# Kernel tuning notes

Hardware: AMD Instinct MI355X
Metric: run time of the kernel (lower is better)

Reference implementation:

```python
import jax, jax.numpy as jnp
import numpy as np

N_NODES = 50000
N_EDGES = 800000
D_IN = 768
D_H = 256
N_CLASSES = 4
N_LAYERS = 3
N_GRAPHS = 64
LN_EPS = 1e-5


def setup_inputs() -> dict:
    key = jax.random.key(0)
    ks = jax.random.split(key, 12)
    x = jax.random.normal(ks[0], (N_NODES, D_IN), dtype=jnp.float32)
    edge_index = jax.random.randint(ks[1], (2, N_EDGES), 0, N_NODES)
    batch = jnp.sort(jax.random.randint(ks[2], (N_NODES,), 0, N_GRAPHS))
    s_in = 1.0 / np.sqrt(D_IN)
    s_h = 1.0 / np.sqrt(D_H)
    W_in = jax.random.normal(ks[3], (D_IN, D_H), jnp.float32) * s_in
    b_in = jnp.zeros((D_H,), jnp.float32)
    convW = jax.random.normal(ks[4], (N_LAYERS, D_H, D_H), jnp.float32) * s_h
    convB = jnp.zeros((N_LAYERS, D_H), jnp.float32)
    lnG = jnp.ones((N_LAYERS, D_H), jnp.float32)
    lnB = jnp.zeros((N_LAYERS, D_H), jnp.float32)
    clsW1 = jax.random.normal(ks[5], (D_H, D_H), jnp.float32) * s_h
    clsB1 = jnp.zeros((D_H,), jnp.float32)
    clsW2 = jax.random.normal(ks[6], (D_H, N_CLASSES), jnp.float32) * s_h
    clsB2 = jnp.zeros((N_CLASSES,), jnp.float32)
    return {"x": x, "edge_index": edge_index, "batch": batch,
            "W_in": W_in, "b_in": b_in, "convW": convW, "convB": convB,
            "lnG": lnG, "lnB": lnB, "clsW1": clsW1, "clsB1": clsB1,
            "clsW2": clsW2, "clsB2": clsB2}


def _layer_norm(h, g, b):
    mu = jnp.mean(h, axis=-1, keepdims=True)
    var = jnp.mean(jnp.square(h - mu), axis=-1, keepdims=True)
    return (h - mu) * jax.lax.rsqrt(var + LN_EPS) * g + b


def reference(x, edge_index, batch, W_in, b_in, convW, convB, lnG, lnB,
              clsW1, clsB1, clsW2, clsB2):
    N = x.shape[0]
    loops = jnp.arange(N)
    src = jnp.concatenate([edge_index[0], loops])  # self-loops (PyG GCNConv default)
    dst = jnp.concatenate([edge_index[1], loops])
    deg = jax.ops.segment_sum(jnp.ones_like(src, dtype=x.dtype), dst, num_segments=N)
    dinv = jax.lax.rsqrt(deg)  # deg >= 1 due to self-loops
    norm = dinv[src] * dinv[dst]  # symmetric GCN normalization per edge

    h = x @ W_in + b_in  # input projection -> [N, D_H]
    for i in range(N_LAYERS):
        m = h @ convW[i]  # transform then propagate
        h_new = jax.ops.segment_sum(m[src] * norm[:, None], dst, num_segments=N) + convB[i]
        h = jax.nn.relu(h_new + h)  # residual (shapes match), then ReLU
        h = _layer_norm(h, lnG[i], lnB[i])
        # dropout: identity (inference mode)

    g = jax.ops.segment_max(h, batch, num_segments=N_GRAPHS)  # global_max_pool
    z = jax.nn.relu(g @ clsW1 + clsB1)
    return z @ clsW2 + clsB2  # [N_GRAPHS, N_CLASSES]
```

## Files before the change

### kernel.cpp

```cpp
#include <hip/hip_runtime.h>
#include <hip/hip_bf16.h>
#include <math.h>

#define NNODES 50000
#define NEDGES 800000
#define DIN 768
#define DH 256
#define NCLS 4
#define NGRAPHS 64
#define SCAN_BLOCKS 196

typedef __bf16 bf16x8 __attribute__((ext_vector_type(8)));
typedef float f32x4 __attribute__((ext_vector_type(4)));

static __device__ __forceinline__ float bf2f(unsigned short u) {
    union { unsigned u32; float f; } v; v.u32 = ((unsigned)u) << 16; return v.f;
}
static __device__ __forceinline__ unsigned short f2bf(float f) {
    union { float f; unsigned u; } v; v.f = f;
    unsigned r = (v.u + 0x7fffu + ((v.u >> 16) & 1u)) >> 16;
    return (unsigned short)r;
}
static __device__ __forceinline__ void unpack8(uint4 u, float* f) {
    f[0] = bf2f((unsigned short)(u.x & 0xffff)); f[1] = bf2f((unsigned short)(u.x >> 16));
    f[2] = bf2f((unsigned short)(u.y & 0xffff)); f[3] = bf2f((unsigned short)(u.y >> 16));
    f[4] = bf2f((unsigned short)(u.z & 0xffff)); f[5] = bf2f((unsigned short)(u.z >> 16));
    f[6] = bf2f((unsigned short)(u.w & 0xffff)); f[7] = bf2f((unsigned short)(u.w >> 16));
}
static __device__ __forceinline__ uint4 pack8f(float4 f0, float4 f1) {
    uint4 u;
    u.x = (unsigned)f2bf(f0.x) | ((unsigned)f2bf(f0.y) << 16);
    u.y = (unsigned)f2bf(f0.z) | ((unsigned)f2bf(f0.w) << 16);
    u.z = (unsigned)f2bf(f1.x) | ((unsigned)f2bf(f1.y) << 16);
    u.w = (unsigned)f2bf(f1.z) | ((unsigned)f2bf(f1.w) << 16);
    return u;
}
static __device__ __forceinline__ void gload_lds16(const void* g, void* l) {
    __builtin_amdgcn_global_load_lds((const __attribute__((address_space(1))) void*)g,
                                     (__attribute__((address_space(3))) void*)l, 16, 0, 0);
}

__global__ void detect_dtype(const unsigned short* __restrict__ x, int* __restrict__ flag) {
    __shared__ int cnt_s;
    if (threadIdx.x == 0) cnt_s = 0;
    __syncthreads();
    int c = 0;
    for (int i = 0; i < 16; ++i) {
        float v = bf2f(x[threadIdx.x * 16 + i]);
        if (!(fabsf(v) < 1e10f)) c++;
    }
    atomicAdd(&cnt_s, c);
    __syncthreads();
    if (threadIdx.x == 0) flag[0] = (cnt_s > 32) ? 1 : 0;
}

static __device__ __forceinline__ unsigned short cload(const void* src, int i, int fp32) {
    return fp32 ? f2bf(((const float*)src)[i]) : ((const unsigned short*)src)[i];
}

__global__ void canon_small(const void* b_in, const void* convB, const void* lnG,
                            const void* lnB, const void* W1, const void* W2,
                            const void* b1, const void* b2,
                            unsigned short* __restrict__ dst, const int* __restrict__ flag) {
    int i = blockIdx.x * 256 + threadIdx.x;
    if (i >= 69380) return;
    const int fp32 = flag[0];
    int j = i;
    if (j < 256)  { dst[i] = cload(b_in, j, fp32); return; }  j -= 256;
    if (j < 768)  { dst[i] = cload(convB, j, fp32); return; } j -= 768;
    if (j < 768)  { dst[i] = cload(lnG, j, fp32); return; }   j -= 768;
    if (j < 768)  { dst[i] = cload(lnB, j, fp32); return; }   j -= 768;
    if (j < 65536){ dst[i] = cload(W1, j, fp32); return; }    j -= 65536;
    if (j < 1024) { dst[i] = cload(W2, j, fp32); return; }    j -= 1024;
    if (j < 256)  { dst[i] = cload(b1, j, fp32); return; }    j -= 256;
    dst[i] = cload(b2, j, fp32);
}

__global__ void transpose_win(const void* __restrict__ src, unsigned short* __restrict__ dst,
                              const int* __restrict__ flag) {
    int idx = blockIdx.x * 256 + threadIdx.x;
    if (idx < DIN * DH) {
        int r = idx / DH, c = idx % DH;
        dst[(size_t)c * DIN + r] = cload(src, idx, flag[0]);
    }
}
__global__ void transpose_convw(const void* __restrict__ src, unsigned short* __restrict__ dst,
                                const int* __restrict__ flag) {
    int idx = blockIdx.x * 256 + threadIdx.x;
    if (idx < 3 * DH * DH) {
        int l = idx >> 16, rc = idx & 65535;
        int r = rc >> 8, c = rc & 255;
        dst[(l << 16) + c * DH + r] = cload(src, idx, flag[0]);
    }
}

__global__ void fill_sentinel(float* out, int n) {
    int i = blockIdx.x * 256 + threadIdx.x;
    if (i < n) out[i] = 1000.0f;
}

__global__ void count_edges(const int* __restrict__ ei, int* __restrict__ cnt) {
    int e = blockIdx.x * 256 + threadIdx.x;
    if (e < NEDGES) atomicAdd(&cnt[ei[NEDGES + e]], 1);
}

__global__ void scan_local(const int* __restrict__ cnt, int* __restrict__ rowptr,
                           int* __restrict__ bsum) {
    __shared__ int tmp[256];
    int i = blockIdx.x * 256 + threadIdx.x;
    int v = (i < NNODES) ? cnt[i] : 0;
    tmp[threadIdx.x] = v;
    __syncthreads();
    for (int off = 1; off < 256; off <<= 1) {
        int a = (threadIdx.x >= off) ? tmp[threadIdx.x - off] : 0;
        __syncthreads();
        tmp[threadIdx.x] += a;
        __syncthreads();
    }
    if (i < NNODES) rowptr[i] = tmp[threadIdx.x] - v;
    if (threadIdx.x == 255) bsum[blockIdx.x] = tmp[255];
}
__global__ void scan_bsum(const int* __restrict__ bsum, int* __restrict__ boff) {
    __shared__ int tmp[256];
    int t = threadIdx.x;
    int v = (t < SCAN_BLOCKS) ? bsum[t] : 0;
    tmp[t] = v;
    __syncthreads();
    for (int off = 1; off < 256; off <<= 1) {
        int a = (t >= off) ? tmp[t - off] : 0;
        __syncthreads();
        tmp[t] += a;
        __syncthreads();
    }
    if (t < SCAN_BLOCKS) boff[t] = tmp[t] - v;
}
__global__ void scan_finish(int* __restrict__ rowptr, const int* __restrict__ boff,
                            const int* __restrict__ cnt, float* __restrict__ dinv) {
    int i = blockIdx.x * 256 + threadIdx.x;
    if (i < NNODES) {
        rowptr[i] += boff[blockIdx.x];
        dinv[i] = rsqrtf((float)(1 + cnt[i]));
    }
    if (i == 0) rowptr[NNODES] = NEDGES;
}

__global__ void fill_csr(const int* __restrict__ ei, const int* __restrict__ rowptr,
                         int* __restrict__ cursor, int* __restrict__ csrc) {
    int e = blockIdx.x * 256 + threadIdx.x;
    if (e < NEDGES) {
        int s = ei[e];
        int d = ei[NEDGES + e];
        int pos = rowptr[d] + atomicAdd(&cursor[d], 1);
        csrc[pos] = s;
    }
}

#define GBM 64
#define GBN 256
#define GBK 32

__global__ __launch_bounds__(256, 3) void gemm_bf16_tn(
    const void* __restrict__ Araw, const int* __restrict__ dflag, int use_flag,
    const unsigned short* __restrict__ Bt, const unsigned short* __restrict__ bias,
    unsigned short* __restrict__ C, int M, int N, int K)
{
    __shared__ __align__(16) unsigned short As[2][GBM * GBK];
    __shared__ __align__(16) unsigned short Bs[2][GBN * GBK];

    const int a_fp32 = use_flag ? dflag[0] : 0;
    const int m0 = blockIdx.x * GBM;
    const int t = threadIdx.x;
    const int wave = t >> 6, lane = t & 63;
    const int quad = lane >> 4, l16 = lane & 15;
    const int qs8 = (quad ^ ((l16 >> 1) & 3)) * 8;

    const int ar = t >> 2;
    const int ap_ = t & 3;
    const int al = ap_ ^ ((ar >> 1) & 3);
    const bool arow_ok = (m0 + ar) < M;
    const float* abase_f = (const float*)Araw + (size_t)(m0 + ar) * K + al * 8;
    const unsigned short* abase_h = (const unsigned short*)Araw + (size_t)(m0 + ar) * K + al * 8;

    const char* bsrcb[4];
#pragma unroll
    for (int li = 0; li < 4; ++li) {
        int c = wave * 256 + li * 64 + lane;
        int r = c >> 2, p = c & 3;
        int l = p ^ ((r >> 1) & 3);
        bsrcb[li] = (const char*)Bt + ((size_t)r * K + l * 8) * 2;
    }

    f32x4 acc[4][4];
#pragma unroll
    for (int i = 0; i < 4; i++)
#pragma unroll
        for (int j = 0; j < 4; j++) acc[i][j] = (f32x4){0.f, 0.f, 0.f, 0.f};

    {
#pragma unroll
        for (int li = 0; li < 4; ++li)
            gload_lds16(bsrcb[li], &Bs[0][(wave * 256 + li * 64) * 8]);
        uint4 av = make_uint4(0u, 0u, 0u, 0u);
        if (arow_ok) {
            if (a_fp32) {
                float4 f0 = *(const float4*)abase_f;
                float4 f1 = *(const float4*)(abase_f + 4);
                av = pack8f(f0, f1);
            } else {
                av = *(const uint4*)abase_h;
            }
        }
        *(uint4*)(&As[0][t * 8]) = av;
    }
    __syncthreads();

    const int nt = K / GBK;
    for (int tt = 0; tt < nt; ++tt) {
        const int buf = tt & 1;
        const bool hn = (tt + 1) < nt;
        uint4 av = make_uint4(0u, 0u, 0u, 0u);
        float4 f0 = make_float4(0.f, 0.f, 0.f, 0.f);
        float4 f1 = make_float4(0.f, 0.f, 0.f, 0.f);
        if (hn) {
            const int kk = (tt + 1) * GBK;
#pragma unroll
            for (int li = 0; li < 4; ++li)
                gload_lds16(bsrcb[li] + (size_t)kk * 2,
                            &Bs[buf ^ 1][(wave * 256 + li * 64) * 8]);
            if (arow_ok) {
                if (a_fp32) {
                    f0 = *(const float4*)(abase_f + kk);
                    f1 = *(const float4*)(abase_f + kk + 4);
                } else {
                    av = *(const uint4*)(abase_h + kk);
                }
            }
        }
        const unsigned short* as_ = As[buf];
        const unsigned short* bs_ = Bs[buf];
        bf16x8 afv[4], bfv[4];
#pragma unroll
        for (int i = 0; i < 4; i++)
            afv[i] = *(const bf16x8*)(as_ + (16 * i + l16) * 32 + qs8);
#pragma unroll
        for (int j = 0; j < 4; j++)
            bfv[j] = *(const bf16x8*)(bs_ + (wave * 64 + 16 * j + l16) * 32 + qs8);
#pragma unroll
        for (int i = 0; i < 4; i++)
#pragma unroll
            for (int j = 0; j < 4; j++)
                acc[i][j] = __builtin_amdgcn_mfma_f32_16x16x32_bf16(afv[i], bfv[j], acc[i][j], 0, 0, 0);
        if (hn) {
            if (a_fp32 && arow_ok) av = pack8f(f0, f1);
            *(uint4*)(&As[buf ^ 1][t * 8]) = av;
        }
        __syncthreads();
    }

#pragma unroll
    for (int j = 0; j < 4; j++) {
        const int gc = wave * 64 + 16 * j + l16;
        const float bv = bias ? bf2f(bias[gc]) : 0.f;
#pragma unroll
        for (int i = 0; i < 4; i++) {
#pragma unroll
            for (int rr = 0; rr < 4; rr++) {
                int gr = m0 + 16 * i + quad * 4 + rr;
                if (gr < M) C[(size_t)gr * N + gc] = f2bf(acc[i][j][rr] + bv);
            }
        }
    }
}

__global__ __launch_bounds__(256) void aggregate_ln(
    const int* __restrict__ rowptr, const int* __restrict__ csrc,
    const float* __restrict__ dinv, const unsigned short* __restrict__ m,
    const unsigned short* __restrict__ convB,
    const unsigned short* __restrict__ lnG, const unsigned short* __restrict__ lnB,
    unsigned short* __restrict__ h)
{
    const int half = threadIdx.x >> 5;
    const int lane = threadIdx.x & 31;
    const int node = blockIdx.x * 8 + half;
    const float di = dinv[node];
    const size_t base = (size_t)node * DH + lane * 8;
    const size_t lo = lane * 8;

    float v0[8], v1[8], v2[8], v3[8];
    unpack8(*(const uint4*)(m + base), v0);
    const float selfn = di * di;
#pragma unroll
    for (int j = 0; j < 8; j++) { v0[j] *= selfn; v1[j] = 0.f; v2[j] = 0.f; v3[j] = 0.f; }

    const int kb = rowptr[node], ke = rowptr[node + 1];
    int k = kb;
    for (; k + 4 <= ke; k += 4) {
        const int s0 = csrc[k], s1 = csrc[k + 1], s2 = csrc[k + 2], s3 = csrc[k + 3];
        const uint4 r0 = *(const uint4*)(m + (size_t)s0 * DH + lo);
        const uint4 r1 = *(const uint4*)(m + (size_t)s1 * DH + lo);
        const uint4 r2 = *(const uint4*)(m + (size_t)s2 * DH + lo);
        const uint4 r3 = *(const uint4*)(m + (size_t)s3 * DH + lo);
        const float n0 = dinv[s0] * di, n1 = dinv[s1] * di;
        const float n2 = dinv[s2] * di, n3 = dinv[s3] * di;
        float t0[8], t1[8], t2[8], t3[8];
        unpack8(r0, t0); unpack8(r1, t1); unpack8(r2, t2); unpack8(r3, t3);
#pragma unroll
        for (int j = 0; j < 8; j++) {
            v0[j] += t0[j] * n0;
            v1[j] += t1[j] * n1;
            v2[j] += t2[j] * n2;
            v3[j] += t3[j] * n3;
        }
    }
    for (; k < ke; ++k) {
        const int s = csrc[k];
        const uint4 r = *(const uint4*)(m + (size_t)s * DH + lo);
        const float n = dinv[s] * di;
        float tv[8];
        unpack8(r, tv);
#pragma unroll
        for (int j = 0; j < 8; j++) v0[j] += tv[j] * n;
    }
#pragma unroll
    for (int j = 0; j < 8; j++) v0[j] += (v1[j] + v2[j]) + v3[j];

    float hv[8], cv[8];
    unpack8(*(const uint4*)(h + base), hv);
    unpack8(*(const uint4*)(convB + lo), cv);
    float s1 = 0.f, s2 = 0.f;
#pragma unroll
    for (int j = 0; j < 8; j++) {
        v0[j] = fmaxf(v0[j] + cv[j] + hv[j], 0.f);
        s1 += v0[j];
        s2 += v0[j] * v0[j];
    }
#pragma unroll
    for (int off = 16; off > 0; off >>= 1) {
        s1 += __shfl_xor(s1, off, 32);
        s2 += __shfl_xor(s2, off, 32);
    }
    const float mu = s1 * (1.f / 256.f);
    const float var = s2 * (1.f / 256.f) - mu * mu;
    const float rs = rsqrtf(var + 1e-5f);
    float gv[8], bv[8];
    unpack8(*(const uint4*)(lnG + lo), gv);
    unpack8(*(const uint4*)(lnB + lo), bv);
    unsigned short o[8];
#pragma unroll
    for (int j = 0; j < 8; j++) o[j] = f2bf((v0[j] - mu) * rs * gv[j] + bv[j]);
    uint4 outp;
    outp.x = (unsigned)o[0] | ((unsigned)o[1] << 16);
    outp.y = (unsigned)o[2] | ((unsigned)o[3] << 16);
    outp.z = (unsigned)o[4] | ((unsigned)o[5] << 16);
    outp.w = (unsigned)o[6] | ((unsigned)o[7] << 16);
    *(uint4*)(h + base) = outp;
}

__global__ void find_bounds(const int* __restrict__ batch, int* __restrict__ s) {
    int i = blockIdx.x * 256 + threadIdx.x;
    if (i >= NNODES) return;
    int b = batch[i];
    int bp = (i == 0) ? -1 : batch[i - 1];
    for (int g = bp + 1; g <= b; ++g) s[g] = i;
    if (i == NNODES - 1)
        for (int g = b + 1; g <= NGRAPHS; ++g) s[g] = NNODES;
}

#define PSPLIT 8
__global__ __launch_bounds__(256) void pool_partial(
    const unsigned short* __restrict__ h, const int* __restrict__ s,
    float* __restrict__ pg)
{
    const int b = blockIdx.x >> 3, split = blockIdx.x & 7, f = threadIdx.x;
    const int i0 = s[b], i1 = s[b + 1];
    const int len = i1 - i0;
    const int c0 = i0 + (int)(((long)len * split) >> 3);
    const int c1 = i0 + (int)(((long)len * (split + 1)) >> 3);
    float mx = -INFINITY;
    for (int i = c0; i < c1; ++i) mx = fmaxf(mx, bf2f(h[(size_t)i * DH + f]));
    pg[(size_t)blockIdx.x * DH + f] = mx;
}
__global__ __launch_bounds__(256) void pool_reduce(const float* __restrict__ pg,
                                                   float* __restrict__ g) {
    const int b = blockIdx.x, f = threadIdx.x;
    float mx = -INFINITY;
#pragma unroll
    for (int j = 0; j < PSPLIT; ++j) mx = fmaxf(mx, pg[(size_t)(b * PSPLIT + j) * DH + f]);
    g[b * DH + f] = mx;
}

__global__ __launch_bounds__(256) void classifier(
    const float* __restrict__ g, const unsigned short* __restrict__ W1,
    const unsigned short* __restrict__ b1, const unsigned short* __restrict__ W2,
    const unsigned short* __restrict__ b2, void* __restrict__ outv,
    const int* __restrict__ flag)
{
    __shared__ float gz[DH];
    __shared__ float zz[DH];
    const int b = blockIdx.x, t = threadIdx.x;
    gz[t] = g[b * DH + t];
    __syncthreads();
    float s = bf2f(b1[t]);
    for (int k = 0; k < DH; ++k) s += gz[k] * bf2f(W1[k * DH + t]);
    zz[t] = fmaxf(s, 0.f);
    __syncthreads();
    if (t < NCLS) {
        float s2 = bf2f(b2[t]);
        for (int k = 0; k < DH; ++k) s2 += zz[k] * bf2f(W2[k * NCLS + t]);
        if (flag[0]) ((float*)outv)[b * NCLS + t] = s2;
        else ((unsigned short*)outv)[b * NCLS + t] = f2bf(s2);
    }
}

extern "C" void kernel_launch(void* const* d_in, const int* in_sizes, int n_in,
                              void* d_out, int out_size, void* d_ws, size_t ws_size,
                              hipStream_t stream)
{
    const void* x      = d_in[0];
    const int* ei      = (const int*)d_in[1];
    const int* batch   = (const int*)d_in[2];
    const void* Win    = d_in[3];
    const void* b_in   = d_in[4];
    const void* convW  = d_in[5];
    const void* convB  = d_in[6];
    const void* lnG    = d_in[7];
    const void* lnB    = d_in[8];
    const void* W1     = d_in[9];
    const void* b1     = d_in[10];
    const void* W2     = d_in[11];
    const void* b2     = d_in[12];

    char* ws = (char*)d_ws;
    unsigned short* h   = (unsigned short*)(ws + 0);
    unsigned short* m   = (unsigned short*)(ws + 25600000);
    int* csrc           = (int*)(ws + 51200000);
    int* rowptr         = (int*)(ws + 54400000);
    int* cnt            = (int*)(ws + 54600016);
    int* cursor         = (int*)(ws + 54800016);
    float* dinv         = (float*)(ws + 55000016);
    unsigned short* cw  = (unsigned short*)(ws + 55200016);
    unsigned short* WinT= (unsigned short*)(ws + 55338784);
    unsigned short* WcT = (unsigned short*)(ws + 55732000);
    float* g            = (float*)(ws + 56125216);
    float* pg           = (float*)(ws + 56190752);
    int* gb             = (int*)(ws + 56715040);
    int* bsum           = (int*)(ws + 56715312);
    int* boff           = (int*)(ws + 56716112);
    int* flag           = (int*)(ws + 56716912);
    const size_t NEED   = 56716928;
    if (ws_size < NEED) {
        fill_sentinel<<<(out_size / 2 + 255) / 256, 256, 0, stream>>>((float*)d_out, out_size / 2);
        return;
    }

    unsigned short* cBin   = cw + 0;
    unsigned short* cConvB = cw + 256;
    unsigned short* cLnG   = cw + 1024;
    unsigned short* cLnB   = cw + 1792;
    unsigned short* cW1    = cw + 2560;
    unsigned short* cW2    = cw + 68096;
    unsigned short* cB1    = cw + 69120;
    unsigned short* cB2    = cw + 69376;

    detect_dtype<<<1, 256, 0, stream>>>((const unsigned short*)x, flag);

    hipMemsetAsync(cnt, 0, 400000, stream);
    count_edges<<<(NEDGES + 255) / 256, 256, 0, stream>>>(ei, cnt);
    scan_local<<<SCAN_BLOCKS, 256, 0, stream>>>(cnt, rowptr, bsum);
    scan_bsum<<<1, 256, 0, stream>>>(bsum, boff);
    scan_finish<<<SCAN_BLOCKS, 256, 0, stream>>>(rowptr, boff, cnt, dinv);
    fill_csr<<<(NEDGES + 255) / 256, 256, 0, stream>>>(ei, rowptr, cursor, csrc);

    canon_small<<<(69380 + 255) / 256, 256, 0, stream>>>(b_in, convB, lnG, lnB, W1, W2, b1, b2, cw, flag);
    transpose_win<<<(DIN * DH + 255) / 256, 256, 0, stream>>>(Win, WinT, flag);
    transpose_convw<<<(3 * DH * DH + 255) / 256, 256, 0, stream>>>(convW, WcT, flag);

    dim3 gg((NNODES + GBM - 1) / GBM, 1);
    gemm_bf16_tn<<<gg, 256, 0, stream>>>(x, flag, 1, WinT, cBin, h, NNODES, DH, DIN);

    for (int i = 0; i < 3; i++) {
        gemm_bf16_tn<<<gg, 256, 0, stream>>>(h, flag, 0, WcT + i * DH * DH, nullptr, m,
                                             NNODES, DH, DH);
        aggregate_ln<<<NNODES / 8, 256, 0, stream>>>(
            rowptr, csrc, dinv, m, cConvB + i * DH, cLnG + i * DH, cLnB + i * DH, h);
    }

    find_bounds<<<(NNODES + 255) / 256, 256, 0, stream>>>(batch, gb);
    pool_partial<<<NGRAPHS * PSPLIT, 256, 0, stream>>>(h, gb, pg);
    pool_reduce<<<NGRAPHS, 256, 0, stream>>>(pg, g);
    classifier<<<NGRAPHS, 256, 0, stream>>>(g, cW1, cB1, cW2, cB2, d_out, flag);
}
```

Measured before the change: 689.4 us.

## Load GEMM A tiles via direct global-to-LDS and template on input dtype

The A operand is now loaded with asynchronous global_load_lds copies instead of register loads followed by LDS stores, using a swizzled layout. For fp32 input the raw floats are staged in LDS and converted to bf16 when fragments are read. The kernel is templated on the fp32 flag so the bf16 variant uses less LDS and can raise occupancy from 3 to 4 blocks. Out-of-range rows are clamped to the last row rather than zero-filled, which is harmless because those rows are never written back.

```diff
diff --git a/kernel.cpp b/kernel.cpp
--- a/kernel.cpp
+++ b/kernel.cpp
@@ -26,14 +26,6 @@
     f[2] = bf2f((unsigned short)(u.y & 0xffff)); f[3] = bf2f((unsigned short)(u.y >> 16));
     f[4] = bf2f((unsigned short)(u.z & 0xffff)); f[5] = bf2f((unsigned short)(u.z >> 16));
     f[6] = bf2f((unsigned short)(u.w & 0xffff)); f[7] = bf2f((unsigned short)(u.w >> 16));
-}
-static __device__ __forceinline__ uint4 pack8f(float4 f0, float4 f1) {
-    uint4 u;
-    u.x = (unsigned)f2bf(f0.x) | ((unsigned)f2bf(f0.y) << 16);
-    u.y = (unsigned)f2bf(f0.z) | ((unsigned)f2bf(f0.w) << 16);
-    u.z = (unsigned)f2bf(f1.x) | ((unsigned)f2bf(f1.y) << 16);
-    u.w = (unsigned)f2bf(f1.z) | ((unsigned)f2bf(f1.w) << 16);
-    return u;
 }
 static __device__ __forceinline__ void gload_lds16(const void* g, void* l) {
     __builtin_amdgcn_global_load_lds((const __attribute__((address_space(1))) void*)g,
@@ -155,39 +147,45 @@
     }
 }
 
-#define GBM 64
-#define GBN 256
-#define GBK 32
-
-__global__ __launch_bounds__(256, 3) void gemm_bf16_tn(
-    const void* __restrict__ Araw, const int* __restrict__ dflag, int use_flag,
+template<int WF>
+__global__ __launch_bounds__(256, WF ? 3 : 4) void gemm_core(
+    const void* __restrict__ Araw, const int* __restrict__ dflag,
     const unsigned short* __restrict__ Bt, const unsigned short* __restrict__ bias,
-    unsigned short* __restrict__ C, int M, int N, int K)
+    unsigned short* __restrict__ C, int M, int K)
 {
-    __shared__ __align__(16) unsigned short As[2][GBM * GBK];
-    __shared__ __align__(16) unsigned short Bs[2][GBN * GBK];
-
-    const int a_fp32 = use_flag ? dflag[0] : 0;
-    const int m0 = blockIdx.x * GBM;
-    const int t = threadIdx.x;
-    const int wave = t >> 6, lane = t & 63;
+    __shared__ __align__(16) char As[2][WF ? 8192 : 4096];
+    __shared__ __align__(16) char Bs[2][16384];
+
+    const int af32 = WF ? dflag[0] : 0;
+    const int m0 = blockIdx.x * 64;
+    const int t = threadIdx.x, wave = t >> 6, lane = t & 63;
     const int quad = lane >> 4, l16 = lane & 15;
-    const int qs8 = (quad ^ ((l16 >> 1) & 3)) * 8;
-
-    const int ar = t >> 2;
-    const int ap_ = t & 3;
-    const int al = ap_ ^ ((ar >> 1) & 3);
-    const bool arow_ok = (m0 + ar) < M;
-    const float* abase_f = (const float*)Araw + (size_t)(m0 + ar) * K + al * 8;
-    const unsigned short* abase_h = (const unsigned short*)Araw + (size_t)(m0 + ar) * K + al * 8;
-
-    const char* bsrcb[4];
+
+    const char* bsrc[4];
 #pragma unroll
     for (int li = 0; li < 4; ++li) {
         int c = wave * 256 + li * 64 + lane;
         int r = c >> 2, p = c & 3;
         int l = p ^ ((r >> 1) & 3);
-        bsrcb[li] = (const char*)Bt + ((size_t)r * K + l * 8) * 2;
+        bsrc[li] = (const char*)Bt + ((size_t)r * K + l * 8) * 2;
+    }
+    const char* asrc[2];
+    if (af32) {
+#pragma unroll
+        for (int li = 0; li < 2; ++li) {
+            int c = wave * 128 + li * 64 + lane;
+            int r = c >> 3, p = c & 7;
+            int l = p ^ (r & 7);
+            int rg = min(m0 + r, M - 1);
+            asrc[li] = (const char*)Araw + ((size_t)rg * K + l * 4) * 4;
+        }
+    } else {
+        int c = wave * 64 + lane;
+        int r = c >> 2, p = c & 3;
+        int l = p ^ ((r >> 1) & 3);
+        int rg = min(m0 + r, M - 1);
+        asrc[0] = (const char*)Araw + ((size_t)rg * K + l * 8) * 2;
+        asrc[1] = asrc[0];
     }
 
     f32x4 acc[4][4];
@@ -199,61 +197,65 @@
     {
 #pragma unroll
         for (int li = 0; li < 4; ++li)
-            gload_lds16(bsrcb[li], &Bs[0][(wave * 256 + li * 64) * 8]);
-        uint4 av = make_uint4(0u, 0u, 0u, 0u);
-        if (arow_ok) {
-            if (a_fp32) {
-                float4 f0 = *(const float4*)abase_f;
-                float4 f1 = *(const float4*)(abase_f + 4);
-                av = pack8f(f0, f1);
-            } else {
-                av = *(const uint4*)abase_h;
-            }
-        }
-        *(uint4*)(&As[0][t * 8]) = av;
-    }
-    __syncthreads();
-
-    const int nt = K / GBK;
+            gload_lds16(bsrc[li], &Bs[0][(wave * 256 + li * 64) * 16]);
+        if (af32) {
+            gload_lds16(asrc[0], &As[0][(wave * 128) * 16]);
+            gload_lds16(asrc[1], &As[0][(wave * 128 + 64) * 16]);
+        } else {
+            gload_lds16(asrc[0], &As[0][(wave * 64) * 16]);
+        }
+    }
+    __syncthreads();
+
+    const int nt = K / 32;
     for (int tt = 0; tt < nt; ++tt) {
         const int buf = tt & 1;
-        const bool hn = (tt + 1) < nt;
-        uint4 av = make_uint4(0u, 0u, 0u, 0u);
-        float4 f0 = make_float4(0.f, 0.f, 0.f, 0.f);
-        float4 f1 = make_float4(0.f, 0.f, 0.f, 0.f);
-        if (hn) {
-            const int kk = (tt + 1) * GBK;
+        if (tt + 1 < nt) {
+            const size_t k0 = (size_t)(tt + 1) * 32;
 #pragma unroll
             for (int li = 0; li < 4; ++li)
-                gload_lds16(bsrcb[li] + (size_t)kk * 2,
-                            &Bs[buf ^ 1][(wave * 256 + li * 64) * 8]);
-            if (arow_ok) {
-                if (a_fp32) {
-                    f0 = *(const float4*)(abase_f + kk);
-                    f1 = *(const float4*)(abase_f + kk + 4);
-                } else {
-                    av = *(const uint4*)(abase_h + kk);
-                }
+                gload_lds16(bsrc[li] + k0 * 2, &Bs[buf ^ 1][(wave * 256 + li * 64) * 16]);
+            if (af32) {
+                gload_lds16(asrc[0] + k0 * 4, &As[buf ^ 1][(wave * 128) * 16]);
+                gload_lds16(asrc[1] + k0 * 4, &As[buf ^ 1][(wave * 128 + 64) * 16]);
+            } else {
+                gload_lds16(asrc[0] + k0 * 2, &As[buf ^ 1][(wave * 64) * 16]);
             }
         }
-        const unsigned short* as_ = As[buf];
-        const unsigned short* bs_ = Bs[buf];
+        const char* as_ = As[buf];
+        const char* bs_ = Bs[buf];
         bf16x8 afv[4], bfv[4];
-#pragma unroll
-        for (int i = 0; i < 4; i++)
-            afv[i] = *(const bf16x8*)(as_ + (16 * i + l16) * 32 + qs8);
-#pragma unroll
-        for (int j = 0; j < 4; j++)
-            bfv[j] = *(const bf16x8*)(bs_ + (wave * 64 + 16 * j + l16) * 32 + qs8);
+        if (af32) {
+#pragma unroll
+            for (int i = 0; i < 4; i++) {
+                const int row = 16 * i + l16;
+                const int ph0 = (quad * 2) ^ (row & 7);
+                float4 x0 = *(const float4*)(as_ + row * 128 + ph0 * 16);
+                float4 x1 = *(const float4*)(as_ + row * 128 + (ph0 ^ 1) * 16);
+                union { bf16x8 v; __bf16 e[8]; } u;
+                u.e[0] = (__bf16)x0.x; u.e[1] = (__bf16)x0.y;
+                u.e[2] = (__bf16)x0.z; u.e[3] = (__bf16)x0.w;
+                u.e[4] = (__bf16)x1.x; u.e[5] = (__bf16)x1.y;
+                u.e[6] = (__bf16)x1.z; u.e[7] = (__bf16)x1.w;
+                afv[i] = u.v;
+            }
+        } else {
+            const int ph = (quad ^ ((l16 >> 1) & 3)) * 16;
+#pragma unroll
+            for (int i = 0; i < 4; i++)
+                afv[i] = *(const bf16x8*)(as_ + (16 * i + l16) * 64 + ph);
+        }
+        {
+            const int ph = (quad ^ ((l16 >> 1) & 3)) * 16;
+#pragma unroll
+            for (int j = 0; j < 4; j++)
+                bfv[j] = *(const bf16x8*)(bs_ + (wave * 64 + 16 * j + l16) * 64 + ph);
+        }
 #pragma unroll
         for (int i = 0; i < 4; i++)
 #pragma unroll
             for (int j = 0; j < 4; j++)
                 acc[i][j] = __builtin_amdgcn_mfma_f32_16x16x32_bf16(afv[i], bfv[j], acc[i][j], 0, 0, 0);
-        if (hn) {
-            if (a_fp32 && arow_ok) av = pack8f(f0, f1);
-            *(uint4*)(&As[buf ^ 1][t * 8]) = av;
-        }
         __syncthreads();
     }
 
@@ -266,7 +268,7 @@
 #pragma unroll
             for (int rr = 0; rr < 4; rr++) {
                 int gr = m0 + 16 * i + quad * 4 + rr;
-                if (gr < M) C[(size_t)gr * N + gc] = f2bf(acc[i][j][rr] + bv);
+                if (gr < M) C[(size_t)gr * 256 + gc] = f2bf(acc[i][j][rr] + bv);
             }
         }
     }
@@ -475,12 +477,12 @@
     transpose_win<<<(DIN * DH + 255) / 256, 256, 0, stream>>>(Win, WinT, flag);
     transpose_convw<<<(3 * DH * DH + 255) / 256, 256, 0, stream>>>(convW, WcT, flag);
 
-    dim3 gg((NNODES + GBM - 1) / GBM, 1);
-    gemm_bf16_tn<<<gg, 256, 0, stream>>>(x, flag, 1, WinT, cBin, h, NNODES, DH, DIN);
+    const int GBLK = (NNODES + 63) / 64;
+    gemm_core<1><<<GBLK, 256, 0, stream>>>(x, flag, WinT, cBin, h, NNODES, DIN);
 
     for (int i = 0; i < 3; i++) {
-        gemm_bf16_tn<<<gg, 256, 0, stream>>>(h, flag, 0, WcT + i * DH * DH, nullptr, m,
-                                             NNODES, DH, DH);
+        gemm_core<0><<<GBLK, 256, 0, stream>>>(h, flag, WcT + i * DH * DH, nullptr, m,
+                                               NNODES, DH);
         aggregate_ln<<<NNODES / 8, 256, 0, stream>>>(
             rowptr, csrc, dinv, m, cConvB + i * DH, cLnG + i * DH, cLnB + i * DH, h);
     }
```

Result: no change. 689.0 us (-0.1%).
